# Kernel optimization log

Hardware: AMD Instinct MI355X
Metric: run time of the kernel (lower is better)

## Reference

```python
import jax, jax.numpy as jnp
import numpy as np

EMBED = 128
NUM_HOPS = 3
VOCAB = 32000
MEM = 50
PAD = 0


def pos_weights(J, d):
    # MemN2N position encoding: 1 - (j+1)/J - (k+1)/d * (1 - 2*(j+1)/J)
    j = jnp.arange(J, dtype=jnp.float32)[:, None]
    k = jnp.arange(d, dtype=jnp.float32)[None, :]
    return 1.0 - (j + 1.0) / J - (k + 1.0) / d * (1.0 - 2.0 * (j + 1.0) / J)


def setup_inputs() -> dict:
    key = jax.random.key(0)
    ks = jax.random.split(key, 10)
    ctx_query = jax.random.randint(ks[0], (16, 10, 20), 0, VOCAB)
    story = jax.random.randint(ks[1], (16, MEM, 40), 0, VOCAB)

    def emb(k):
        w = 0.1 * jax.random.normal(k, (VOCAB, EMBED), dtype=jnp.float32)
        return w.at[PAD].set(0.0)  # padding_idx row is zero

    A_w = emb(ks[2])
    C_w = emb(ks[3])
    B_w = emb(ks[4])
    H_w = 0.1 * jax.random.normal(ks[5], (EMBED, EMBED), dtype=jnp.float32)
    H_b = 0.1 * jax.random.normal(ks[6], (EMBED,), dtype=jnp.float32)
    out_w = 0.1 * jax.random.normal(ks[7], (VOCAB, EMBED), dtype=jnp.float32)
    TA = 0.1 * jax.random.normal(ks[8], (MEM, EMBED), dtype=jnp.float32)
    TC = 0.1 * jax.random.normal(ks[9], (MEM, EMBED), dtype=jnp.float32)
    return {"ctx_query": ctx_query, "story": story, "A_w": A_w, "C_w": C_w,
            "B_w": B_w, "H_w": H_w, "H_b": H_b, "out_w": out_w, "TA": TA, "TC": TC}


def reference(ctx_query, story, A_w, C_w, B_w, H_w, H_b, out_w, TA, TC):
    B, NQ, S = ctx_query.shape
    R, S2 = story.shape[1], story.shape[2]
    cq = ctx_query.reshape(B * NQ, S)
    # story repeated across num_qa (broadcast instead of materialized repeat)
    st = jnp.broadcast_to(story[:, None], (B, NQ, R, S2)).reshape(B * NQ, R, S2)

    qw = pos_weights(S, EMBED)            # [S, d]
    state = jnp.sum(B_w[cq] * qw, axis=1)  # [BN, d]

    sw = pos_weights(S2, EMBED)           # [S2, d]
    for _ in range(NUM_HOPS):             # use_lw=True: A/C tied across hops
        mem = jnp.sum(A_w[st] * sw, axis=2) + TA    # [BN, R, d]
        outm = jnp.sum(C_w[st] * sw, axis=2) + TC   # [BN, R, d]
        probs = jax.nn.softmax(jnp.einsum('brd,bd->br', mem, state), axis=-1)
        response = jnp.einsum('br,brd->bd', probs, outm)  # [BN, d]
        state = response @ H_w.T + H_b + state      # H(response) + state
    return state @ out_w.T                          # [BN, vocab]
```

## Files before the change

### kernel.cpp

```cpp
#include <hip/hip_runtime.h>
#include <hip/hip_bf16.h>
#include <math.h>

#define EMBED 128
#define VOCAB 32000
#define MEMN  50
#define BATCH 16
#define NQ    10
#define SQ    20
#define SS    40
#define BN    (BATCH*NQ)
#define NHOPS 3
#define NV    64

typedef short v8s __attribute__((ext_vector_type(8)));
typedef float v4f __attribute__((ext_vector_type(4)));

__device__ __forceinline__ float posw(int j, int J, int k) {
    float jf = (float)(j + 1) / (float)J;
    return 1.0f - jf - ((float)(k + 1) / (float)EMBED) * (1.0f - 2.0f * jf);
}

__device__ __forceinline__ short f2bf(float f) {
    __hip_bfloat16 h = __float2bfloat16(f);
    return *(short*)&h;
}

__global__ void k_embed(const int* __restrict__ cq, const int* __restrict__ story,
                        const float* __restrict__ Bw, const float* __restrict__ Aw,
                        const float* __restrict__ Cw, const float* __restrict__ TA,
                        const float* __restrict__ TC, const float* __restrict__ Hw,
                        float* __restrict__ state, float* __restrict__ memb,
                        float* __restrict__ outb, float* __restrict__ HwT) {
    int blk = blockIdx.x;
    int t = threadIdx.x;
    if (blk < BN) {
        float acc = 0.f;
        #pragma unroll
        for (int s = 0; s < SQ; ++s) {
            int tok = cq[blk * SQ + s];
            acc += Bw[tok * EMBED + t] * posw(s, SQ, t);
        }
        state[blk * EMBED + t] = acc;
    } else if (blk < BN + BATCH * MEMN) {
        int br = blk - BN;
        int r = br % MEMN;
        float ma = TA[r * EMBED + t];
        float mc = TC[r * EMBED + t];
        const int* toks = story + br * SS;
        #pragma unroll 4
        for (int s = 0; s < SS; ++s) {
            int tok = toks[s];
            float w = posw(s, SS, t);
            ma += Aw[tok * EMBED + t] * w;
            mc += Cw[tok * EMBED + t] * w;
        }
        memb[br * EMBED + t] = ma;
        outb[br * EMBED + t] = mc;
    } else {
        int k = blk - (BN + BATCH * MEMN);
        HwT[k * EMBED + t] = Hw[t * EMBED + k];
    }
}

__global__ void k_hops(const float* __restrict__ memb, const float* __restrict__ outb,
                       const float* __restrict__ HwT, const float* __restrict__ Hb,
                       const float* __restrict__ state, __hip_bfloat16* __restrict__ stateb) {
    __shared__ float lmem[MEMN][EMBED + 1];
    __shared__ float lout[MEMN][EMBED + 1];
    __shared__ float lstate[EMBED];
    __shared__ float lprobs[MEMN];
    __shared__ float lresp[EMBED];
    int bn = blockIdx.x;
    int b  = bn / NQ;
    int t  = threadIdx.x;
    for (int i = t; i < MEMN * EMBED; i += EMBED) {
        int r = i >> 7, d = i & 127;
        lmem[r][d] = memb[b * MEMN * EMBED + i];
        lout[r][d] = outb[b * MEMN * EMBED + i];
    }
    lstate[t] = state[bn * EMBED + t];
    __syncthreads();

    for (int hop = 0; hop < NHOPS; ++hop) {
        float logit = -1e30f;
        if (t < MEMN) {
            float acc = 0.f;
            for (int d = 0; d < EMBED; ++d) acc += lmem[t][d] * lstate[d];
            logit = acc;
        }
        if (t < 64) {
            float m = logit;
            #pragma unroll
            for (int off = 32; off; off >>= 1) m = fmaxf(m, __shfl_xor(m, off, 64));
            float e = (t < MEMN) ? __expf(logit - m) : 0.f;
            float ssum = e;
            #pragma unroll
            for (int off = 32; off; off >>= 1) ssum += __shfl_xor(ssum, off, 64);
            if (t < MEMN) lprobs[t] = e / ssum;
        }
        __syncthreads();
        float resp = 0.f;
        for (int r = 0; r < MEMN; ++r) resp += lprobs[r] * lout[r][t];
        lresp[t] = resp;
        __syncthreads();
        float acc = Hb[t] + lstate[t];
        for (int k = 0; k < EMBED; ++k) acc += lresp[k] * HwT[k * EMBED + t];
        __syncthreads();
        lstate[t] = acc;
        __syncthreads();
    }
    stateb[bn * EMBED + t] = __float2bfloat16(lstate[t]);
}

__global__ __launch_bounds__(256) void k_out(const __hip_bfloat16* __restrict__ stateb,
                                             const float* __restrict__ outw,
                                             float* __restrict__ out) {
    __shared__ __align__(16) __hip_bfloat16 Alds[BN][EMBED + 8];
    __shared__ __align__(16) __hip_bfloat16 Blds[NV][EMBED + 8];
    int t = threadIdx.x;
    int vbase = blockIdx.x * NV;

    #pragma unroll
    for (int i = 0; i < 10; ++i) {
        int e = t + i * 256;
        int row = e >> 4, c8 = (e & 15) << 3;
        *(int4*)&Alds[row][c8] = *(const int4*)&stateb[row * EMBED + c8];
    }
    #pragma unroll
    for (int i = 0; i < 8; ++i) {
        int e = t + i * 256;
        int row = e >> 5, c4 = (e & 31) << 2;
        float4 w = *(const float4*)&outw[(size_t)(vbase + row) * EMBED + c4];
        short4 p;
        p.x = f2bf(w.x); p.y = f2bf(w.y); p.z = f2bf(w.z); p.w = f2bf(w.w);
        *(short4*)&Blds[row][c4] = p;
    }
    __syncthreads();

    int wv = t >> 6;
    int l = t & 63;
    int col16 = l & 15;
    int kg = l >> 4;

    v8s bfrag[4];
    #pragma unroll
    for (int k4 = 0; k4 < 4; ++k4)
        bfrag[k4] = *(v8s*)&Blds[(wv << 4) + col16][k4 * 32 + kg * 8];

    v4f acc[10];
    #pragma unroll
    for (int m = 0; m < 10; ++m) acc[m] = (v4f){0.f, 0.f, 0.f, 0.f};

    #pragma unroll
    for (int k4 = 0; k4 < 4; ++k4) {
        #pragma unroll
        for (int m = 0; m < 10; ++m) {
            v8s af = *(v8s*)&Alds[m * 16 + col16][k4 * 32 + kg * 8];
            acc[m] = __builtin_amdgcn_mfma_f32_16x16x32_bf16(af, bfrag[k4], acc[m], 0, 0, 0);
        }
    }

    int colg = vbase + (wv << 4) + col16;
    #pragma unroll
    for (int m = 0; m < 10; ++m) {
        #pragma unroll
        for (int i = 0; i < 4; ++i) {
            out[(size_t)(m * 16 + kg * 4 + i) * VOCAB + colg] = acc[m][i];
        }
    }
}

extern "C" void kernel_launch(void* const* d_in, const int* in_sizes, int n_in,
                              void* d_out, int out_size, void* d_ws, size_t ws_size,
                              hipStream_t stream) {
    const int*   ctx_query = (const int*)  d_in[0];
    const int*   story     = (const int*)  d_in[1];
    const float* A_w       = (const float*)d_in[2];
    const float* C_w       = (const float*)d_in[3];
    const float* B_w       = (const float*)d_in[4];
    const float* H_w       = (const float*)d_in[5];
    const float* H_b       = (const float*)d_in[6];
    const float* out_w     = (const float*)d_in[7];
    const float* TA        = (const float*)d_in[8];
    const float* TC        = (const float*)d_in[9];
    float* out = (float*)d_out;

    float* ws    = (float*)d_ws;
    float* state = ws;
    float* memb  = state + BN * EMBED;
    float* outb  = memb + BATCH * MEMN * EMBED;
    float* HwT   = outb + BATCH * MEMN * EMBED;
    __hip_bfloat16* stateb = (__hip_bfloat16*)(HwT + EMBED * EMBED);

    k_embed<<<BN + BATCH * MEMN + EMBED, EMBED, 0, stream>>>(
        ctx_query, story, B_w, A_w, C_w, TA, TC, H_w, state, memb, outb, HwT);
    k_hops<<<BN, EMBED, 0, stream>>>(memb, outb, HwT, H_b, state, stateb);
    k_out<<<VOCAB / NV, 256, 0, stream>>>(stateb, out_w, out);
}
```

Before: 35.39 us.

## Rewrite hop loop as per-batch MFMA kernel with split-bf16 precision

The hop kernel now runs one block per batch of 10 queries instead of one per query, so each batch's memory rows are loaded once and shared across its questions. The logits, response and H projections run on bf16 MFMA using hi/lo splitting (three products each) to keep roughly fp32 accuracy. LDS tiles are XOR-swizzled to avoid bank conflicts, and H_w is pre-split into bf16 hi/lo instead of being transposed. This replaces scalar per-thread dot products with matrix instructions, at the cost of only 16 blocks and extra conversion work.

```diff
diff --git a/kernel.cpp b/kernel.cpp
--- a/kernel.cpp
+++ b/kernel.cpp
@@ -16,6 +16,8 @@
 typedef short v8s __attribute__((ext_vector_type(8)));
 typedef float v4f __attribute__((ext_vector_type(4)));
 
+#define MFMA16 __builtin_amdgcn_mfma_f32_16x16x32_bf16
+
 __device__ __forceinline__ float posw(int j, int J, int k) {
     float jf = (float)(j + 1) / (float)J;
     return 1.0f - jf - ((float)(k + 1) / (float)EMBED) * (1.0f - 2.0f * jf);
@@ -24,6 +26,10 @@
 __device__ __forceinline__ short f2bf(float f) {
     __hip_bfloat16 h = __float2bfloat16(f);
     return *(short*)&h;
+}
+__device__ __forceinline__ float bf2f(short s) {
+    __hip_bfloat16 h = *(__hip_bfloat16*)&s;
+    return __bfloat162float(h);
 }
 
 __global__ void k_embed(const int* __restrict__ cq, const int* __restrict__ story,
@@ -31,7 +37,8 @@
                         const float* __restrict__ Cw, const float* __restrict__ TA,
                         const float* __restrict__ TC, const float* __restrict__ Hw,
                         float* __restrict__ state, float* __restrict__ memb,
-                        float* __restrict__ outb, float* __restrict__ HwT) {
+                        float* __restrict__ outb, short* __restrict__ HwBhi,
+                        short* __restrict__ HwBlo) {
     int blk = blockIdx.x;
     int t = threadIdx.x;
     if (blk < BN) {
@@ -58,59 +65,190 @@
         memb[br * EMBED + t] = ma;
         outb[br * EMBED + t] = mc;
     } else {
-        int k = blk - (BN + BATCH * MEMN);
-        HwT[k * EMBED + t] = Hw[t * EMBED + k];
-    }
-}
-
-__global__ void k_hops(const float* __restrict__ memb, const float* __restrict__ outb,
-                       const float* __restrict__ HwT, const float* __restrict__ Hb,
-                       const float* __restrict__ state, __hip_bfloat16* __restrict__ stateb) {
-    __shared__ float lmem[MEMN][EMBED + 1];
-    __shared__ float lout[MEMN][EMBED + 1];
-    __shared__ float lstate[EMBED];
-    __shared__ float lprobs[MEMN];
-    __shared__ float lresp[EMBED];
-    int bn = blockIdx.x;
-    int b  = bn / NQ;
-    int t  = threadIdx.x;
-    for (int i = t; i < MEMN * EMBED; i += EMBED) {
-        int r = i >> 7, d = i & 127;
-        lmem[r][d] = memb[b * MEMN * EMBED + i];
-        lout[r][d] = outb[b * MEMN * EMBED + i];
-    }
-    lstate[t] = state[bn * EMBED + t];
+        int row = blk - (BN + BATCH * MEMN);
+        float v = Hw[row * EMBED + t];
+        short h = f2bf(v);
+        HwBhi[row * EMBED + t] = h;
+        HwBlo[row * EMBED + t] = f2bf(v - bf2f(h));
+    }
+}
+
+__global__ __launch_bounds__(256) void k_hops(const float* __restrict__ memb,
+                                              const float* __restrict__ outb,
+                                              const short* __restrict__ HwBhi,
+                                              const short* __restrict__ HwBlo,
+                                              const float* __restrict__ Hb,
+                                              const float* __restrict__ state,
+                                              __hip_bfloat16* __restrict__ stateb) {
+    __shared__ short mem_hi[64][128], mem_lo[64][128];
+    __shared__ short outT_hi[128][64], outT_lo[128][64];
+    __shared__ short P_hi[16][64], P_lo[16][64];
+    __shared__ short resp_hi[16][128], resp_lo[16][128];
+    __shared__ float stateM[16][132];
+    __shared__ float Lg[16][64];
+    __shared__ float Hb_l[128];
+
+    int b = blockIdx.x;
+    int t = threadIdx.x;
+    int w = t >> 6;
+    int l = t & 63;
+    int c16 = l & 15;
+    int kg = l >> 4;
+
+    {
+        v8s z = {0,0,0,0,0,0,0,0};
+        for (int i = t; i < 64*128/8; i += 256) { ((v8s*)mem_hi)[i] = z; ((v8s*)mem_lo)[i] = z; }
+        for (int i = t; i < 128*64/8; i += 256) { ((v8s*)outT_hi)[i] = z; ((v8s*)outT_lo)[i] = z; }
+        for (int i = t; i < 16*64/8;  i += 256) { ((v8s*)P_hi)[i] = z; ((v8s*)P_lo)[i] = z; }
+        for (int i = t; i < 16*132;   i += 256) ((float*)stateM)[i] = 0.f;
+    }
     __syncthreads();
 
+    {
+        const float4* mb4 = (const float4*)(memb + (size_t)b * MEMN * EMBED);
+        const float4* ob4 = (const float4*)(outb + (size_t)b * MEMN * EMBED);
+        for (int i = t; i < MEMN * EMBED / 4; i += 256) {
+            int r = i >> 5, c4 = (i & 31) << 2;
+            float4 v = mb4[i];
+            float4 u = ob4[i];
+            float mv[4] = {v.x, v.y, v.z, v.w};
+            float ov[4] = {u.x, u.y, u.z, u.w};
+            #pragma unroll
+            for (int j = 0; j < 4; ++j) {
+                int k = c4 + j;
+                short h = f2bf(mv[j]);
+                int pos = (((k >> 3) ^ (r & 15)) << 3) | (k & 7);
+                mem_hi[r][pos] = h;
+                mem_lo[r][pos] = f2bf(mv[j] - bf2f(h));
+                short g = f2bf(ov[j]);
+                int posT = (((r >> 3) ^ (k & 7)) << 3) | (r & 7);
+                outT_hi[k][posT] = g;
+                outT_lo[k][posT] = f2bf(ov[j] - bf2f(g));
+            }
+        }
+        for (int i = t; i < NQ * EMBED; i += 256) {
+            int q = i >> 7, d = i & 127;
+            stateM[q][d] = state[((size_t)b * NQ + q) * EMBED + d];
+        }
+        if (t < 128) Hb_l[t] = Hb[t];
+    }
+    __syncthreads();
+
     for (int hop = 0; hop < NHOPS; ++hop) {
-        float logit = -1e30f;
-        if (t < MEMN) {
-            float acc = 0.f;
-            for (int d = 0; d < EMBED; ++d) acc += lmem[t][d] * lstate[d];
-            logit = acc;
-        }
-        if (t < 64) {
-            float m = logit;
-            #pragma unroll
-            for (int off = 32; off; off >>= 1) m = fmaxf(m, __shfl_xor(m, off, 64));
-            float e = (t < MEMN) ? __expf(logit - m) : 0.f;
-            float ssum = e;
-            #pragma unroll
-            for (int off = 32; off; off >>= 1) ssum += __shfl_xor(ssum, off, 64);
-            if (t < MEMN) lprobs[t] = e / ssum;
+        {
+            v4f acc = {0.f, 0.f, 0.f, 0.f};
+            int mrow = (w << 4) + c16;
+            #pragma unroll
+            for (int ks = 0; ks < 4; ++ks) {
+                float4 s0 = *(const float4*)&stateM[c16][ks*32 + kg*8];
+                float4 s1 = *(const float4*)&stateM[c16][ks*32 + kg*8 + 4];
+                float sv[8] = {s0.x, s0.y, s0.z, s0.w, s1.x, s1.y, s1.z, s1.w};
+                v8s ah, al;
+                #pragma unroll
+                for (int j = 0; j < 8; ++j) {
+                    short h = f2bf(sv[j]);
+                    ah[j] = h;
+                    al[j] = f2bf(sv[j] - bf2f(h));
+                }
+                int pos = ((ks*4 + kg) ^ (mrow & 15)) << 3;
+                v8s bh = *(const v8s*)&mem_hi[mrow][pos];
+                v8s bl = *(const v8s*)&mem_lo[mrow][pos];
+                acc = MFMA16(ah, bh, acc, 0, 0, 0);
+                acc = MFMA16(al, bh, acc, 0, 0, 0);
+                acc = MFMA16(ah, bl, acc, 0, 0, 0);
+            }
+            #pragma unroll
+            for (int i = 0; i < 4; ++i) Lg[kg*4 + i][(w << 4) + c16] = acc[i];
         }
         __syncthreads();
-        float resp = 0.f;
-        for (int r = 0; r < MEMN; ++r) resp += lprobs[r] * lout[r][t];
-        lresp[t] = resp;
+        for (int q = w; q < NQ; q += 4) {
+            float v = (l < MEMN) ? Lg[q][l] : -1e30f;
+            float mx = v;
+            #pragma unroll
+            for (int off = 32; off; off >>= 1) mx = fmaxf(mx, __shfl_xor(mx, off, 64));
+            float e = (l < MEMN) ? __expf(v - mx) : 0.f;
+            float ss = e;
+            #pragma unroll
+            for (int off = 32; off; off >>= 1) ss += __shfl_xor(ss, off, 64);
+            if (l < MEMN) {
+                float p = e / ss;
+                short h = f2bf(p);
+                int pos = (((l >> 3) ^ (q & 7)) << 3) | (l & 7);
+                P_hi[q][pos] = h;
+                P_lo[q][pos] = f2bf(p - bf2f(h));
+            }
+        }
         __syncthreads();
-        float acc = Hb[t] + lstate[t];
-        for (int k = 0; k < EMBED; ++k) acc += lresp[k] * HwT[k * EMBED + t];
+        {
+            v8s ph[2], pl[2];
+            #pragma unroll
+            for (int ks = 0; ks < 2; ++ks) {
+                int pos = ((ks*4 + kg) ^ (c16 & 7)) << 3;
+                ph[ks] = *(const v8s*)&P_hi[c16][pos];
+                pl[ks] = *(const v8s*)&P_lo[c16][pos];
+            }
+            #pragma unroll
+            for (int tile = 0; tile < 2; ++tile) {
+                int d = (w << 4) + tile * 64;
+                int orow = d + c16;
+                v4f acc = {0.f, 0.f, 0.f, 0.f};
+                #pragma unroll
+                for (int ks = 0; ks < 2; ++ks) {
+                    int pos = ((ks*4 + kg) ^ (orow & 7)) << 3;
+                    v8s bh = *(const v8s*)&outT_hi[orow][pos];
+                    v8s bl = *(const v8s*)&outT_lo[orow][pos];
+                    acc = MFMA16(ph[ks], bh, acc, 0, 0, 0);
+                    acc = MFMA16(pl[ks], bh, acc, 0, 0, 0);
+                    acc = MFMA16(ph[ks], bl, acc, 0, 0, 0);
+                }
+                #pragma unroll
+                for (int i = 0; i < 4; ++i) {
+                    int row = kg*4 + i, col = d + c16;
+                    float v = acc[i];
+                    short h = f2bf(v);
+                    int pos = (((col >> 3) ^ (row & 15)) << 3) | (col & 7);
+                    resp_hi[row][pos] = h;
+                    resp_lo[row][pos] = f2bf(v - bf2f(h));
+                }
+            }
+        }
         __syncthreads();
-        lstate[t] = acc;
+        {
+            v8s rh[4], rl[4];
+            #pragma unroll
+            for (int ks = 0; ks < 4; ++ks) {
+                int pos = ((ks*4 + kg) ^ (c16 & 15)) << 3;
+                rh[ks] = *(const v8s*)&resp_hi[c16][pos];
+                rl[ks] = *(const v8s*)&resp_lo[c16][pos];
+            }
+            #pragma unroll
+            for (int tile = 0; tile < 2; ++tile) {
+                int d = (w << 4) + tile * 64;
+                int hrow = d + c16;
+                const v8s* gh = (const v8s*)(HwBhi + (size_t)hrow * EMBED);
+                const v8s* gl = (const v8s*)(HwBlo + (size_t)hrow * EMBED);
+                v4f acc = {0.f, 0.f, 0.f, 0.f};
+                #pragma unroll
+                for (int ks = 0; ks < 4; ++ks) {
+                    v8s bh = gh[ks*4 + kg];
+                    v8s bl = gl[ks*4 + kg];
+                    acc = MFMA16(rh[ks], bh, acc, 0, 0, 0);
+                    acc = MFMA16(rl[ks], bh, acc, 0, 0, 0);
+                    acc = MFMA16(rh[ks], bl, acc, 0, 0, 0);
+                }
+                #pragma unroll
+                for (int i = 0; i < 4; ++i) {
+                    int row = kg*4 + i, col = d + c16;
+                    stateM[row][col] = acc[i] + Hb_l[col] + stateM[row][col];
+                }
+            }
+        }
         __syncthreads();
     }
-    stateb[bn * EMBED + t] = __float2bfloat16(lstate[t]);
+    for (int i = t; i < NQ * EMBED; i += 256) {
+        int q = i >> 7, d = i & 127;
+        stateb[((size_t)b * NQ + q) * EMBED + d] = __float2bfloat16(stateM[q][d]);
+    }
 }
 
 __global__ __launch_bounds__(256) void k_out(const __hip_bfloat16* __restrict__ stateb,
@@ -157,7 +295,7 @@
         #pragma unroll
         for (int m = 0; m < 10; ++m) {
             v8s af = *(v8s*)&Alds[m * 16 + col16][k4 * 32 + kg * 8];
-            acc[m] = __builtin_amdgcn_mfma_f32_16x16x32_bf16(af, bfrag[k4], acc[m], 0, 0, 0);
+            acc[m] = MFMA16(af, bfrag[k4], acc[m], 0, 0, 0);
         }
     }
 
@@ -190,11 +328,12 @@
     float* state = ws;
     float* memb  = state + BN * EMBED;
     float* outb  = memb + BATCH * MEMN * EMBED;
-    float* HwT   = outb + BATCH * MEMN * EMBED;
-    __hip_bfloat16* stateb = (__hip_bfloat16*)(HwT + EMBED * EMBED);
-
-    k_embed<<<BN + BATCH * MEMN + EMBED, EMBED, 0, stream>>>(
-        ctx_query, story, B_w, A_w, C_w, TA, TC, H_w, state, memb, outb, HwT);
-    k_hops<<<BN, EMBED, 0, stream>>>(memb, outb, HwT, H_b, state, stateb);
+    short* HwBhi = (short*)(outb + BATCH * MEMN * EMBED);
+    short* HwBlo = HwBhi + EMBED * EMBED;
+    __hip_bfloat16* stateb = (__hip_bfloat16*)(HwBlo + EMBED * EMBED);
+
+    k_embed<<<BN + BATCH * MEMN + EMBED, 128, 0, stream>>>(
+        ctx_query, story, B_w, A_w, C_w, TA, TC, H_w, state, memb, outb, HwBhi, HwBlo);
+    k_hops<<<BATCH, 256, 0, stream>>>(memb, outb, HwBhi, HwBlo, H_b, state, stateb);
     k_out<<<VOCAB / NV, 256, 0, stream>>>(stateb, out_w, out);
 }
```

Measured after the change: 36.89 us. +4.2%, slower.
